# Performance work log

Hardware: AMD Instinct MI355X
Metric: run time of the kernel (lower is better)

## Reference

```python
import jax, jax.numpy as jnp
import numpy as np

EPS = 1e-6
LAMB = 0.05
NEG = -1000.0


def setup_inputs() -> dict:
    key = jax.random.key(0)
    k1, k2, k3, k4, k5, k6 = jax.random.split(key, 6)
    Bi, Bt, K, L, D = 128, 128, 36, 64, 1024
    imgs = jax.random.normal(k1, (Bi, K, D), dtype=jnp.float32)
    caps = jax.random.normal(k2, (Bt, L, D), dtype=jnp.float32)
    img_cls = jax.random.normal(k3, (Bi, D), dtype=jnp.float32)
    cap_cls = jax.random.normal(k4, (Bt, D), dtype=jnp.float32)
    # variable lengths; pin one element to max so torch's [:, :max] slice is identity
    img_lens = jax.random.randint(k5, (Bi,), K // 2, K + 1).astype(jnp.int32).at[0].set(K)
    cap_lens = jax.random.randint(k6, (Bt,), L // 2, L + 1).astype(jnp.int32).at[0].set(L)
    return {"img_cls": img_cls, "imgs": imgs, "cap_cls": cap_cls,
            "caps": caps, "img_lens": img_lens, "cap_lens": cap_lens}


def reference(img_cls, imgs, cap_cls, caps, img_lens, cap_lens):
    # HiCHAN.forward_cam (img_cls / cap_cls unused by this branch)
    imgs = imgs + EPS
    caps = caps + EPS
    imgs = imgs / jnp.linalg.norm(imgs, axis=-1, keepdims=True)
    caps = caps / jnp.linalg.norm(caps, axis=-1, keepdims=True)

    K, L = imgs.shape[1], caps.shape[1]
    # fine-grained similarity tensor [Bi, Bt, K, L]
    fg_sims = jnp.einsum('ikd,tld->itkl', imgs, caps)

    # fg mask: valid region k of image i AND valid word l of caption t
    img_valid = jnp.arange(K)[None, :] < img_lens[:, None]      # [Bi, K]
    cap_valid = jnp.arange(L)[None, :] < cap_lens[:, None]      # [Bt, L]
    mask = img_valid[:, None, :, None] & cap_valid[None, :, None, :]  # [Bi,Bt,K,L] bool
    m = mask.astype(fg_sims.dtype)

    # masked temperature softmax (single scores tensor reused for both axes)
    scores = jnp.where(mask, fg_sims, NEG) / LAMB
    v2t_attn = jax.nn.softmax(scores, axis=-1)
    v2t = jnp.sum(v2t_attn * fg_sims * m, axis=-1)   # [Bi,Bt,K]
    t2v_attn = jax.nn.softmax(scores, axis=-2)
    t2v = jnp.sum(t2v_attn * fg_sims * m, axis=-2)   # [Bi,Bt,L]

    # _ave_init: uniform weights over valid rows / cols
    r_b = mask.any(axis=-1).astype(fg_sims.dtype)    # [Bi,Bt,K]
    c_b = mask.any(axis=-2).astype(fg_sims.dtype)    # [Bi,Bt,L]
    r = r_b / r_b.sum(axis=-1, keepdims=True)
    c = c_b / c_b.sum(axis=-1, keepdims=True)

    sims = (jnp.sum(v2t * r, axis=-1) + jnp.sum(t2v * c, axis=-1)) / 2  # [Bi,Bt]
    return sims
```

## Files before the change

kernel.cpp:

```cpp
#include <hip/hip_runtime.h>
#include <stdint.h>

#define BI 128
#define BT 128
#define KIMG 36
#define LCAP 64
#define DD 1024
#define MP 48
#define MB 96
#define NB 256
#define ASLOTS 384
#define ABYTES 6144
#define STG_BYTES 22528

typedef _Float16 h4 __attribute__((ext_vector_type(4)));
typedef _Float16 h8 __attribute__((ext_vector_type(8)));
typedef float f4 __attribute__((ext_vector_type(4)));

__device__ __forceinline__ float wave_red_sum(float v) {
#pragma unroll
  for (int o = 1; o < 64; o <<= 1) v += __shfl_xor(v, o, 64);
  return v;
}
__device__ __forceinline__ float wave_red_max(float v) {
#pragma unroll
  for (int o = 1; o < 64; o <<= 1) v = fmaxf(v, __shfl_xor(v, o, 64));
  return v;
}

__global__ __launch_bounds__(256) void norm_kernel(
    const float* __restrict__ imgs, const float* __restrict__ caps,
    _Float16* __restrict__ Ah, _Float16* __restrict__ Bh) {
  int row = blockIdx.x;
  int tid = threadIdx.x;
  const float* src;
  _Float16* dst;
  if (row < BI * MP) {
    int i = row / MP, k = row - i * MP;
    dst = Ah + (size_t)row * DD;
    if (k >= KIMG) {
      h4 z = {};
      ((h4*)dst)[tid] = z;
      return;
    }
    src = imgs + ((size_t)i * KIMG + k) * DD;
  } else {
    int r = row - BI * MP;
    dst = Bh + (size_t)r * DD;
    src = caps + (size_t)r * DD;
  }
  float4 x = ((const float4*)src)[tid];
  x.x += 1e-6f; x.y += 1e-6f; x.z += 1e-6f; x.w += 1e-6f;
  float ss = x.x * x.x + x.y * x.y + x.z * x.z + x.w * x.w;
  ss = wave_red_sum(ss);
  __shared__ float red[4];
  int lane = tid & 63, w = tid >> 6;
  if (lane == 0) red[w] = ss;
  __syncthreads();
  float scale = rsqrtf(red[0] + red[1] + red[2] + red[3]);
  h4 o;
  o[0] = (_Float16)(x.x * scale);
  o[1] = (_Float16)(x.y * scale);
  o[2] = (_Float16)(x.z * scale);
  o[3] = (_Float16)(x.w * scale);
  ((h4*)dst)[tid] = o;
}

__global__ __launch_bounds__(256, 2) void sims_kernel(
    const _Float16* __restrict__ Ah, const _Float16* __restrict__ Bh,
    const int* __restrict__ img_lens, const int* __restrict__ cap_lens,
    float* __restrict__ out) {
  __shared__ char stage[3 * STG_BYTES] __attribute__((aligned(16)));

  int tid = threadIdx.x;
  int lane = tid & 63;
  int w = tid >> 6;
  int bx = blockIdx.x;
  int by = blockIdx.y;
  int fr = lane & 15;
  int fq = lane >> 4;

  const size_t arow0 = (size_t)by * MB;
  const size_t brow0 = (size_t)bx * NB;

  int c0 = 6 * w - ((w >> 1) & (w & 1));
  int nch = (w < 2) ? 6 : 5;
  int s0 = c0 * 64 + lane;
  bool isA = (w == 0);
  int srel = isA ? s0 : s0 - ASLOTS;
  int sw0 = srel ^ ((srel >> 3) & 7);
  const _Float16* gp0 =
      (isA ? Ah + arow0 * DD : Bh + brow0 * DD) + (size_t)(sw0 >> 2) * DD + (sw0 & 3) * 8;
  const int lds0 = c0 * 1024 + lane * 16;

  int aoff[6], boff[4];
#pragma unroll
  for (int mi = 0; mi < 6; ++mi) {
    int s = (16 * mi + fr) * 4 + fq;
    aoff[mi] = (s ^ ((s >> 3) & 7)) * 16;
  }
#pragma unroll
  for (int ni = 0; ni < 4; ++ni) {
    int s = (64 * w + 16 * ni + fr) * 4 + fq;
    boff[ni] = ABYTES + (s ^ ((s >> 3) & 7)) * 16;
  }

  auto STAGE = [&](int buf, int k0) {
#pragma unroll
    for (int it = 0; it < 6; ++it) {
      if (it < nch) {
        __builtin_amdgcn_global_load_lds(
            (const __attribute__((address_space(1))) void*)(gp0 + (size_t)it * 16 * DD + k0),
            (__attribute__((address_space(3))) void*)(stage + buf * STG_BYTES + lds0 + it * 1024),
            16, 0, 0);
      }
    }
  };

  f4 acc[6][4] = {};

  STAGE(0, 0);
  STAGE(1, 32);

  for (int t = 0; t < 32; ++t) {
    if (t == 31) {
      asm volatile("s_waitcnt vmcnt(0)" ::: "memory");
    } else if (w < 2) {
      asm volatile("s_waitcnt vmcnt(6)" ::: "memory");
    } else {
      asm volatile("s_waitcnt vmcnt(5)" ::: "memory");
    }
    __builtin_amdgcn_s_barrier();
    __builtin_amdgcn_sched_barrier(0);

    if (t < 30) STAGE((t + 2) % 3, 32 * (t + 2));

    const char* rb = stage + (t % 3) * STG_BYTES;
    h8 af[6], bf[4];
#pragma unroll
    for (int mi = 0; mi < 6; ++mi)
      af[mi] = *(const h8*)(rb + aoff[mi]);
#pragma unroll
    for (int ni = 0; ni < 4; ++ni)
      bf[ni] = *(const h8*)(rb + boff[ni]);
#pragma unroll
    for (int mi = 0; mi < 6; ++mi)
#pragma unroll
      for (int ni = 0; ni < 4; ++ni)
        acc[mi][ni] = __builtin_amdgcn_mfma_f32_16x16x32_f16(
            af[mi], bf[ni], acc[mi][ni], 0, 0, 0);
  }

  int t = bx * 4 + w;
  int Lt = cap_lens[t];

#pragma unroll
  for (int img = 0; img < 2; ++img) {
    int Ki = img_lens[2 * by + img];

    float m = -1e30f;
#pragma unroll
    for (int mi = 0; mi < 3; ++mi)
#pragma unroll
      for (int ni = 0; ni < 4; ++ni)
#pragma unroll
        for (int j = 0; j < 4; ++j) {
          bool valid = (16 * mi + 4 * fq + j < Ki) && (16 * ni + fr < Lt);
          if (valid) m = fmaxf(m, acc[3 * img + mi][ni][j]);
        }
    m = wave_red_max(m);

    float rowe[3][4] = {}, rowes[3][4] = {}, cole[4] = {}, coles[4] = {};
#pragma unroll
    for (int mi = 0; mi < 3; ++mi)
#pragma unroll
      for (int ni = 0; ni < 4; ++ni)
#pragma unroll
        for (int j = 0; j < 4; ++j) {
          float s = acc[3 * img + mi][ni][j];
          bool valid = (16 * mi + 4 * fq + j < Ki) && (16 * ni + fr < Lt);
          float e = valid ? __expf((s - m) * 20.0f) : 0.f;
          float es = e * s;
          rowe[mi][j] += e;
          rowes[mi][j] += es;
          cole[ni] += e;
          coles[ni] += es;
        }

    float part = 0.f;
#pragma unroll
    for (int mi = 0; mi < 3; ++mi)
#pragma unroll
      for (int j = 0; j < 4; ++j) {
        float Re = rowe[mi][j], Res = rowes[mi][j];
#pragma unroll
        for (int o = 1; o < 16; o <<= 1) {
          Re += __shfl_xor(Re, o, 64);
          Res += __shfl_xor(Res, o, 64);
        }
        int row = 16 * mi + 4 * fq + j;
        if (fr == 0 && row < Ki) part += (Res / Re) * (0.5f / (float)Ki);
      }
#pragma unroll
    for (int ni = 0; ni < 4; ++ni) {
      float Ce = cole[ni], Ces = coles[ni];
#pragma unroll
      for (int o = 16; o < 64; o <<= 1) {
        Ce += __shfl_xor(Ce, o, 64);
        Ces += __shfl_xor(Ces, o, 64);
      }
      int l = 16 * ni + fr;
      if (fq == 0 && l < Lt) part += (Ces / Ce) * (0.5f / (float)Lt);
    }
    float sim = wave_red_sum(part);
    if (lane == 0) out[(size_t)(2 * by + img) * BT + t] = sim;
  }
}

extern "C" void kernel_launch(void* const* d_in, const int* in_sizes, int n_in,
                              void* d_out, int out_size, void* d_ws, size_t ws_size,
                              hipStream_t stream) {
  const float* imgs = (const float*)d_in[1];
  const float* caps = (const float*)d_in[3];
  const int* img_lens = (const int*)d_in[4];
  const int* cap_lens = (const int*)d_in[5];
  float* out = (float*)d_out;

  _Float16* Ah = (_Float16*)d_ws;
  _Float16* Bh = Ah + (size_t)BI * MP * DD;

  norm_kernel<<<BI * MP + BT * LCAP, 256, 0, stream>>>(imgs, caps, Ah, Bh);
  sims_kernel<<<dim3(BT / 4, BI / 2), 256, 0, stream>>>(Ah, Bh, img_lens, cap_lens, out);
}
```

Before: 160.5 us.

## Double-buffer LDS fragment reads and interleave them with MFMAs

Restructures the GEMM main loop so each step's fragments are read from LDS into registers one iteration ahead. Those reads are interleaved between the MFMA groups of the current step, and s_setprio raises wave priority during the MFMA bursts. The goal is to hide LDS read latency behind matrix math instead of stalling before each MFMA batch. In exchange it doubles fragment register use and now waits for vmcnt(0) at every step, so a global load issued only one step earlier may be exposed.

Result: no change. 159.0 us (-0.9%).

```diff
diff --git a/kernel.cpp b/kernel.cpp
--- a/kernel.cpp
+++ b/kernel.cpp
@@ -118,38 +118,72 @@
   };
 
   f4 acc[6][4] = {};
+  h8 afA[6], bfA[4], afB[6], bfB[4];
+
+  auto READF = [&](const char* rb, h8 (&af)[6], h8 (&bf)[4]) {
+#pragma unroll
+    for (int mi = 0; mi < 6; ++mi) af[mi] = *(const h8*)(rb + aoff[mi]);
+#pragma unroll
+    for (int ni = 0; ni < 4; ++ni) bf[ni] = *(const h8*)(rb + boff[ni]);
+  };
+
+  auto STEP = [&](int t, h8 (&afc)[6], h8 (&bfc)[4], h8 (&afn)[6], h8 (&bfn)[4]) {
+    asm volatile("s_waitcnt vmcnt(0)" ::: "memory");
+    __builtin_amdgcn_s_barrier();
+    STAGE((t + 2) % 3, 32 * (t + 2));
+    const char* rb = stage + ((t + 1) % 3) * STG_BYTES;
+    __builtin_amdgcn_s_setprio(1);
+    afn[0] = *(const h8*)(rb + aoff[0]);
+    afn[1] = *(const h8*)(rb + aoff[1]);
+    afn[2] = *(const h8*)(rb + aoff[2]);
+#pragma unroll
+    for (int mi = 0; mi < 6; ++mi)
+      acc[mi][0] = __builtin_amdgcn_mfma_f32_16x16x32_f16(afc[mi], bfc[0], acc[mi][0], 0, 0, 0);
+    afn[3] = *(const h8*)(rb + aoff[3]);
+    afn[4] = *(const h8*)(rb + aoff[4]);
+    afn[5] = *(const h8*)(rb + aoff[5]);
+#pragma unroll
+    for (int mi = 0; mi < 6; ++mi)
+      acc[mi][1] = __builtin_amdgcn_mfma_f32_16x16x32_f16(afc[mi], bfc[1], acc[mi][1], 0, 0, 0);
+    bfn[0] = *(const h8*)(rb + boff[0]);
+    bfn[1] = *(const h8*)(rb + boff[1]);
+#pragma unroll
+    for (int mi = 0; mi < 6; ++mi)
+      acc[mi][2] = __builtin_amdgcn_mfma_f32_16x16x32_f16(afc[mi], bfc[2], acc[mi][2], 0, 0, 0);
+    bfn[2] = *(const h8*)(rb + boff[2]);
+    bfn[3] = *(const h8*)(rb + boff[3]);
+#pragma unroll
+    for (int mi = 0; mi < 6; ++mi)
+      acc[mi][3] = __builtin_amdgcn_mfma_f32_16x16x32_f16(afc[mi], bfc[3], acc[mi][3], 0, 0, 0);
+    __builtin_amdgcn_s_setprio(0);
+  };
+
+  auto MFMA_ONLY = [&](h8 (&afc)[6], h8 (&bfc)[4]) {
+    __builtin_amdgcn_s_setprio(1);
+#pragma unroll
+    for (int mi = 0; mi < 6; ++mi)
+#pragma unroll
+      for (int ni = 0; ni < 4; ++ni)
+        acc[mi][ni] = __builtin_amdgcn_mfma_f32_16x16x32_f16(afc[mi], bfc[ni], acc[mi][ni], 0, 0, 0);
+    __builtin_amdgcn_s_setprio(0);
+  };
 
   STAGE(0, 0);
   STAGE(1, 32);
-
-  for (int t = 0; t < 32; ++t) {
-    if (t == 31) {
-      asm volatile("s_waitcnt vmcnt(0)" ::: "memory");
-    } else if (w < 2) {
-      asm volatile("s_waitcnt vmcnt(6)" ::: "memory");
-    } else {
-      asm volatile("s_waitcnt vmcnt(5)" ::: "memory");
-    }
-    __builtin_amdgcn_s_barrier();
-    __builtin_amdgcn_sched_barrier(0);
-
-    if (t < 30) STAGE((t + 2) % 3, 32 * (t + 2));
-
-    const char* rb = stage + (t % 3) * STG_BYTES;
-    h8 af[6], bf[4];
-#pragma unroll
-    for (int mi = 0; mi < 6; ++mi)
-      af[mi] = *(const h8*)(rb + aoff[mi]);
-#pragma unroll
-    for (int ni = 0; ni < 4; ++ni)
-      bf[ni] = *(const h8*)(rb + boff[ni]);
-#pragma unroll
-    for (int mi = 0; mi < 6; ++mi)
-#pragma unroll
-      for (int ni = 0; ni < 4; ++ni)
-        acc[mi][ni] = __builtin_amdgcn_mfma_f32_16x16x32_f16(
-            af[mi], bf[ni], acc[mi][ni], 0, 0, 0);
-  }
+  if (w < 2) asm volatile("s_waitcnt vmcnt(6)" ::: "memory");
+  else       asm volatile("s_waitcnt vmcnt(5)" ::: "memory");
+  __builtin_amdgcn_s_barrier();
+  READF(stage, afA, bfA);
+
+  for (int t = 0; t < 30; t += 2) {
+    STEP(t, afA, bfA, afB, bfB);
+    STEP(t + 1, afB, bfB, afA, bfA);
+  }
+  asm volatile("s_waitcnt vmcnt(0)" ::: "memory");
+  __builtin_amdgcn_s_barrier();
+  READF(stage + (31 % 3) * STG_BYTES, afB, bfB);
+  MFMA_ONLY(afA, bfA);
+  MFMA_ONLY(afB, bfB);
 
   int t = bx * 4 + w;
   int Lt = cap_lens[t];
```

## Load B operands directly to registers and stage only A through LDS

Applied to the files above, without the earlier changes.

The B (caption) tile is no longer staged through shared memory. Each wave reads its own 64 B rows straight from global memory into registers, double-buffered one k-step ahead, while only the shared A tile goes through a 3-buffer LDS ring via global_load_lds. The main loop is unrolled by six so buffer indices are static, and the MFMA block is wrapped in s_setprio. The aim is to cut LDS footprint and LDS read traffic, which may raise occupancy. In exchange, B loads become direct global reads with a smaller 16-byte-per-lane access pattern that could expose memory latency.

Result: slower. 185.1 us (+15.3%).

```diff
diff --git a/kernel.cpp b/kernel.cpp
--- a/kernel.cpp
+++ b/kernel.cpp
@@ -9,9 +9,7 @@
 #define MP 48
 #define MB 96
 #define NB 256
-#define ASLOTS 384
-#define ABYTES 6144
-#define STG_BYTES 22528
+#define ABUF 6144
 
 typedef _Float16 h4 __attribute__((ext_vector_type(4)));
 typedef _Float16 h8 __attribute__((ext_vector_type(8)));
@@ -70,7 +68,7 @@
     const _Float16* __restrict__ Ah, const _Float16* __restrict__ Bh,
     const int* __restrict__ img_lens, const int* __restrict__ cap_lens,
     float* __restrict__ out) {
-  __shared__ char stage[3 * STG_BYTES] __attribute__((aligned(16)));
+  __shared__ char stage[3 * ABUF] __attribute__((aligned(16)));
 
   int tid = threadIdx.x;
   int lane = tid & 63;
@@ -83,73 +81,89 @@
   const size_t arow0 = (size_t)by * MB;
   const size_t brow0 = (size_t)bx * NB;
 
-  int c0 = 6 * w - ((w >> 1) & (w & 1));
-  int nch = (w < 2) ? 6 : 5;
+  const int c0 = (w < 2) ? 2 * w : w + 2;
+  const int nch = (w < 2) ? 2 : 1;
   int s0 = c0 * 64 + lane;
-  bool isA = (w == 0);
-  int srel = isA ? s0 : s0 - ASLOTS;
-  int sw0 = srel ^ ((srel >> 3) & 7);
-  const _Float16* gp0 =
-      (isA ? Ah + arow0 * DD : Bh + brow0 * DD) + (size_t)(sw0 >> 2) * DD + (sw0 & 3) * 8;
+  int sw0 = s0 ^ ((s0 >> 3) & 7);
+  const _Float16* gpA = Ah + (arow0 + (sw0 >> 2)) * DD + (sw0 & 3) * 8;
   const int lds0 = c0 * 1024 + lane * 16;
 
-  int aoff[6], boff[4];
-#pragma unroll
-  for (int mi = 0; mi < 6; ++mi) {
-    int s = (16 * mi + fr) * 4 + fq;
-    aoff[mi] = (s ^ ((s >> 3) & 7)) * 16;
-  }
-#pragma unroll
-  for (int ni = 0; ni < 4; ++ni) {
-    int s = (64 * w + 16 * ni + fr) * 4 + fq;
-    boff[ni] = ABYTES + (s ^ ((s >> 3) & 7)) * 16;
-  }
+  int sl = 4 * fr + fq;
+  const int aoff0 = (sl ^ ((sl >> 3) & 7)) * 16;
+
+  const _Float16* bp0 = Bh + (brow0 + 64 * w + fr) * DD + fq * 8;
+  const _Float16* bp1 = bp0 + 16 * DD;
+  const _Float16* bp2 = bp0 + 32 * DD;
+  const _Float16* bp3 = bp0 + 48 * DD;
+
+  f4 acc[6][4] = {};
+  h8 bfA[4], bfB[4];
 
   auto STAGE = [&](int buf, int k0) {
-#pragma unroll
-    for (int it = 0; it < 6; ++it) {
-      if (it < nch) {
-        __builtin_amdgcn_global_load_lds(
-            (const __attribute__((address_space(1))) void*)(gp0 + (size_t)it * 16 * DD + k0),
-            (__attribute__((address_space(3))) void*)(stage + buf * STG_BYTES + lds0 + it * 1024),
-            16, 0, 0);
-      }
-    }
-  };
-
-  f4 acc[6][4] = {};
-
-  STAGE(0, 0);
-  STAGE(1, 32);
-
-  for (int t = 0; t < 32; ++t) {
-    if (t == 31) {
-      asm volatile("s_waitcnt vmcnt(0)" ::: "memory");
-    } else if (w < 2) {
-      asm volatile("s_waitcnt vmcnt(6)" ::: "memory");
-    } else {
-      asm volatile("s_waitcnt vmcnt(5)" ::: "memory");
-    }
+    __builtin_amdgcn_global_load_lds(
+        (const __attribute__((address_space(1))) void*)(gpA + k0),
+        (__attribute__((address_space(3))) void*)(stage + buf * ABUF + lds0), 16, 0, 0);
+    if (nch == 2)
+      __builtin_amdgcn_global_load_lds(
+          (const __attribute__((address_space(1))) void*)(gpA + 16 * DD + k0),
+          (__attribute__((address_space(3))) void*)(stage + buf * ABUF + lds0 + 1024), 16, 0, 0);
+  };
+  auto LOADB = [&](h8(&bf)[4], int k0) {
+    bf[0] = *(const h8*)(bp0 + k0);
+    bf[1] = *(const h8*)(bp1 + k0);
+    bf[2] = *(const h8*)(bp2 + k0);
+    bf[3] = *(const h8*)(bp3 + k0);
+  };
+  auto COMPUTE = [&](int bufR, h8(&bf)[4]) {
+    const char* rb = stage + bufR * ABUF;
+    h8 af[6];
+#pragma unroll
+    for (int mi = 0; mi < 6; ++mi) af[mi] = *(const h8*)(rb + aoff0 + 1024 * mi);
+    __builtin_amdgcn_s_setprio(1);
+#pragma unroll
+    for (int mi = 0; mi < 6; ++mi)
+#pragma unroll
+      for (int ni = 0; ni < 4; ++ni)
+        acc[mi][ni] = __builtin_amdgcn_mfma_f32_16x16x32_f16(af[mi], bf[ni], acc[mi][ni], 0, 0, 0);
+    __builtin_amdgcn_s_setprio(0);
+  };
+  auto WAITN = [&]() {
+    if (w < 2) asm volatile("s_waitcnt vmcnt(2)" ::: "memory");
+    else       asm volatile("s_waitcnt vmcnt(1)" ::: "memory");
+  };
+  auto BODY = [&](int t, int bufR, int bufW, h8(&cur)[4], h8(&nxt)[4]) {
+    LOADB(nxt, 32 * (t + 1));
+    __builtin_amdgcn_sched_barrier(0);
+    STAGE(bufW, 32 * (t + 2));
+    __builtin_amdgcn_sched_barrier(0);
+    COMPUTE(bufR, cur);
+    WAITN();
     __builtin_amdgcn_s_barrier();
     __builtin_amdgcn_sched_barrier(0);
-
-    if (t < 30) STAGE((t + 2) % 3, 32 * (t + 2));
-
-    const char* rb = stage + (t % 3) * STG_BYTES;
-    h8 af[6], bf[4];
-#pragma unroll
-    for (int mi = 0; mi < 6; ++mi)
-      af[mi] = *(const h8*)(rb + aoff[mi]);
-#pragma unroll
-    for (int ni = 0; ni < 4; ++ni)
-      bf[ni] = *(const h8*)(rb + boff[ni]);
-#pragma unroll
-    for (int mi = 0; mi < 6; ++mi)
-#pragma unroll
-      for (int ni = 0; ni < 4; ++ni)
-        acc[mi][ni] = __builtin_amdgcn_mfma_f32_16x16x32_f16(
-            af[mi], bf[ni], acc[mi][ni], 0, 0, 0);
+  };
+
+  STAGE(0, 0);
+  LOADB(bfA, 0);
+  STAGE(1, 32);
+  WAITN();
+  __builtin_amdgcn_s_barrier();
+  __builtin_amdgcn_sched_barrier(0);
+
+  for (int tb = 0; tb < 30; tb += 6) {
+    BODY(tb + 0, 0, 2, bfA, bfB);
+    BODY(tb + 1, 1, 0, bfB, bfA);
+    BODY(tb + 2, 2, 1, bfA, bfB);
+    BODY(tb + 3, 0, 2, bfB, bfA);
+    BODY(tb + 4, 1, 0, bfA, bfB);
+    BODY(tb + 5, 2, 1, bfB, bfA);
   }
+  LOADB(bfB, 32 * 31);
+  __builtin_amdgcn_sched_barrier(0);
+  COMPUTE(0, bfA);
+  asm volatile("s_waitcnt vmcnt(0)" ::: "memory");
+  __builtin_amdgcn_s_barrier();
+  __builtin_amdgcn_sched_barrier(0);
+  COMPUTE(1, bfB);
 
   int t = bx * 4 + w;
   int Lt = cap_lens[t];
```
